# Kernel optimization log

Measured on AMD Instinct MI355X. Metric: run time of the kernel, lower is better.

Reference implementation:

```python
import jax, jax.numpy as jnp
import numpy as np

N = 50000; E = 800000; D_IN = 64; EDGE_D = 1
EMB_H = 128; H = 4; C = 32; HC = H * C; G = 8


def _ln(h, g, b):
    mu = jnp.mean(h, axis=-1, keepdims=True)
    var = jnp.var(h, axis=-1, keepdims=True)
    return (h - mu) * jax.lax.rsqrt(var + 1e-5) * g + b


def _tconv(x, src, dst, ea, wq, bq, wk, bk, wv, bv, we, ws, bs):
    # PyG TransformerConv (beta=False, root_weight=True, concat=True, dropout=0)
    n = x.shape[0]
    q = (x @ wq + bq).reshape(n, H, C)
    k = (x @ wk + bk).reshape(n, H, C)
    v = (x @ wv + bv).reshape(n, H, C)
    e = (ea @ we).reshape(-1, H, C)          # [E,H,C] edge embedding (no bias)
    ke = k[src] + e
    ve = v[src] + e
    logit = jnp.einsum('ehc,ehc->eh', q[dst], ke) / np.float32(np.sqrt(C))
    m = jax.ops.segment_max(logit, dst, num_segments=n)
    m = jnp.where(jnp.isfinite(m), m, 0.0)
    a = jnp.exp(logit - m[dst])
    s = jax.ops.segment_sum(a, dst, num_segments=n)
    alpha = a / (s[dst] + 1e-16)             # softmax over in-edges of each dst
    out = jax.ops.segment_sum(alpha[..., None] * ve, dst, num_segments=n)
    out = out.reshape(n, HC)                 # concat heads
    return out + x @ ws + bs                 # root/skip connection


def _embed(x, src, dst, ea, w1, b1, lng, lnb, w2, b2):
    # EmbedConv: per-edge MLP on [x_j || edge_attr], sum-aggregate to dst.
    # LayerNorm params are SHARED (same nn.LayerNorm instance reused in torch).
    msg = jnp.concatenate([x[src], ea], axis=1) @ w1 + b1
    msg = _ln(jax.nn.relu(msg), lng, lnb)
    msg = _ln(jax.nn.relu(msg @ w2 + b2), lng, lnb)
    return jax.ops.segment_sum(msg, dst, num_segments=x.shape[0])


def _forward(x, edge_attr, params, edge_index, batch_idx):
    src, dst = edge_index[0], edge_index[1]
    h = _embed(x, src, dst, edge_attr, *params[0:6])
    h = jax.nn.relu(_tconv(h, src, dst, edge_attr, *params[6:15]))
    h = jax.nn.relu(_tconv(h, src, dst, edge_attr, *params[15:24]))
    # global mean pool
    s = jax.ops.segment_sum(h, batch_idx, num_segments=G)
    cnt = jax.ops.segment_sum(jnp.ones((h.shape[0],), h.dtype), batch_idx, num_segments=G)
    return s / jnp.maximum(cnt, 1.0)[:, None]


def setup_inputs() -> dict:
    key = jax.random.key(0)
    ks = jax.random.split(key, 40)
    w = lambda k, shp: jax.random.normal(k, shp, dtype=jnp.float32) * 0.05
    inp = {}
    inp['x'] = jax.random.normal(ks[0], (N, D_IN), dtype=jnp.float32)
    inp['edge_index'] = jax.random.randint(ks[1], (2, E), 0, N)
    inp['edge_attr'] = jax.random.uniform(ks[2], (E, EDGE_D), dtype=jnp.float32)
    inp['batch_idx'] = jnp.sort(jax.random.randint(ks[3], (N,), 0, G))
    inp['emb_lin1_w'] = w(ks[4], (D_IN + EDGE_D, EMB_H))
    inp['emb_lin1_b'] = jnp.zeros((EMB_H,), jnp.float32)
    inp['emb_ln_g'] = jnp.ones((EMB_H,), jnp.float32)
    inp['emb_ln_b'] = jnp.zeros((EMB_H,), jnp.float32)
    inp['emb_lin2_w'] = w(ks[5], (EMB_H, EMB_H))
    inp['emb_lin2_b'] = jnp.zeros((EMB_H,), jnp.float32)
    i = 6
    for pre, din in (('g1', EMB_H), ('g2', HC)):
        inp[pre + '_wq'] = w(ks[i], (din, HC)); inp[pre + '_bq'] = jnp.zeros((HC,), jnp.float32)
        inp[pre + '_wk'] = w(ks[i + 1], (din, HC)); inp[pre + '_bk'] = jnp.zeros((HC,), jnp.float32)
        inp[pre + '_wv'] = w(ks[i + 2], (din, HC)); inp[pre + '_bv'] = jnp.zeros((HC,), jnp.float32)
        inp[pre + '_we'] = w(ks[i + 3], (EDGE_D, HC))
        inp[pre + '_ws'] = w(ks[i + 4], (din, HC)); inp[pre + '_bs'] = jnp.zeros((HC,), jnp.float32)
        i += 5
    return inp


def reference(x, edge_index, edge_attr, batch_idx,
              emb_lin1_w, emb_lin1_b, emb_ln_g, emb_ln_b, emb_lin2_w, emb_lin2_b,
              g1_wq, g1_bq, g1_wk, g1_bk, g1_wv, g1_bv, g1_we, g1_ws, g1_bs,
              g2_wq, g2_bq, g2_wk, g2_bk, g2_wv, g2_bv, g2_we, g2_ws, g2_bs):
    params = (emb_lin1_w, emb_lin1_b, emb_ln_g, emb_ln_b, emb_lin2_w, emb_lin2_b,
              g1_wq, g1_bq, g1_wk, g1_bk, g1_wv, g1_bv, g1_we, g1_ws, g1_bs,
              g2_wq, g2_bq, g2_wk, g2_bk, g2_wv, g2_bv, g2_we, g2_ws, g2_bs)
    return _forward(x, edge_attr, params, edge_index, batch_idx)
```

## Files before the change

### kernel.cpp

```cpp
#include <hip/hip_runtime.h>

typedef unsigned short u16;
typedef unsigned int u32;
typedef __attribute__((ext_vector_type(8))) short bf16x8;
typedef __attribute__((ext_vector_type(4))) float f32x4;
typedef __attribute__((ext_vector_type(4))) u32 u32x4;

#define N_NODES 50000
#define N_EDGES 800000

__device__ __forceinline__ float bf2f(u16 u) {
    union { u32 i; float f; } v; v.i = ((u32)u) << 16; return v.f;
}
__device__ __forceinline__ u16 f2bf(float f) {
    union { u32 i; float f; } v; v.f = f;
    u32 i = v.i;
    return (u16)((i + 0x7FFFu + ((i >> 16) & 1u)) >> 16);
}
__device__ __forceinline__ float ldf(const void* p, int i, int fl) {
    return fl ? ((const float*)p)[i] : bf2f(((const u16*)p)[i]);
}
__device__ __forceinline__ int getflag(const int* flag) {
    return __builtin_amdgcn_readfirstlane(*flag);
}

struct P8 { const void* s[8]; };

__global__ __launch_bounds__(256) void k_deg_detect(
    const int* __restrict__ dst, int* __restrict__ cnt,
    const u16* __restrict__ xr, int* __restrict__ flag)
{
    int t = threadIdx.x;
    if (blockIdx.x < 3125) {
        int e = blockIdx.x * 256 + t;
        atomicAdd(&cnt[dst[e]], 1);
        return;
    }
    __shared__ int sc[256];
    int c = 0;
    for (int i = t; i < 4096; i += 256) {
        u32 e = (xr[i] >> 7) & 0xFF;
        if (e >= 143) c++;
    }
    sc[t] = c;
    __syncthreads();
    for (int s = 128; s > 0; s >>= 1) {
        if (t < s) sc[t] += sc[t + s];
        __syncthreads();
    }
    if (t == 0) *flag = (sc[0] > 64) ? 1 : 0;
}

__global__ __launch_bounds__(256) void k_prep_all(
    P8 pw, P8 pb, u16* __restrict__ wcat1, u16* __restrict__ wcat2,
    float* __restrict__ bcat1, float* __restrict__ bcat2,
    const void* __restrict__ w2, const void* __restrict__ lng_,
    const void* __restrict__ lnb_, const void* __restrict__ b2_,
    const void* __restrict__ w1, u16* __restrict__ gt,
    float* __restrict__ csum, float* __restrict__ bwp,
    u32* __restrict__ w1pk, const int* __restrict__ flag)
{
    int fl = getflag(flag);
    int b = blockIdx.x, t = threadIdx.x;
    if (b < 512) {
        int gid = b * 256 + t;
        int wi = gid >> 14;
        int id = gid & 16383;
        int k = id >> 7, n = id & 127;
        u16* d = (wi < 4) ? (wcat1 + wi * 16384) : (wcat2 + (wi - 4) * 16384);
        d[n * 128 + k] = f2bf(ldf(pw.s[wi], id, fl));
    } else if (b < 516) {
        int tt = (b - 512) * 256 + t;
        float v = ldf(pb.s[tt >> 7], tt & 127, fl);
        if (tt < 512) bcat1[tt] = v; else bcat2[tt - 512] = v;
    } else {
        if (t < 128) {
            float cs = 0.f, bw = 0.f;
            for (int f = 0; f < 128; f++) {
                float wv = ldf(w2, f * 128 + t, fl);
                float g = ldf(lng_, f, fl);
                float bb = ldf(lnb_, f, fl);
                u16 gwq = f2bf(g * wv);
                gt[t * 128 + f] = gwq;
                cs += bf2f(gwq);
                bw = fmaf(bb, wv, bw);
            }
            csum[t] = cs;
            bwp[t] = bw + ldf(b2_, t, fl);
            if (t < 64)
                w1pk[t] = (u32)f2bf(ldf(w1, 64 * 128 + t * 2, fl)) |
                          ((u32)f2bf(ldf(w1, 64 * 128 + t * 2 + 1, fl)) << 16);
        }
    }
}

__global__ __launch_bounds__(1024) void k_scan(const int* __restrict__ cnt,
                                               int* __restrict__ row_start,
                                               int* __restrict__ nxt)
{
    __shared__ int wsum[16];
    __shared__ int s_tot;
    int t = threadIdx.x, lane = t & 63, wid = t >> 6;
    int run = 0;
    for (int base = 0; base < N_NODES; base += 8192) {
        int i0 = base + t * 8;
        int v[8], pre[8];
        int s = 0;
        #pragma unroll
        for (int j = 0; j < 8; j++) {
            int i = i0 + j;
            v[j] = (i < N_NODES) ? cnt[i] : 0;
            pre[j] = s;
            s += v[j];
        }
        int tsum = s;
        int sc = tsum;
        #pragma unroll
        for (int off = 1; off < 64; off <<= 1) {
            int o = __shfl_up(sc, off);
            if (lane >= off) sc += o;
        }
        if (lane == 63) wsum[wid] = sc;
        __syncthreads();
        if (t == 0) {
            int acc2 = 0;
            #pragma unroll
            for (int k2 = 0; k2 < 16; k2++) { int vv = wsum[k2]; wsum[k2] = acc2; acc2 += vv; }
            s_tot = acc2;
        }
        __syncthreads();
        int texcl = run + wsum[wid] + (sc - tsum);
        #pragma unroll
        for (int j = 0; j < 8; j++) {
            int i = i0 + j;
            if (i < N_NODES) { int ex = texcl + pre[j]; row_start[i] = ex; nxt[i] = ex; }
        }
        run += s_tot;
        __syncthreads();
    }
    if (t == 0) row_start[N_NODES] = run;
}

__global__ __launch_bounds__(256) void k_lin1_scatter(
    const void* __restrict__ x, const void* __restrict__ w1,
    const void* __restrict__ b1, u16* __restrict__ y,
    const int* __restrict__ dst, const int* __restrict__ srcp,
    const void* __restrict__ ea, int* __restrict__ nxt,
    int2* __restrict__ csr, const int* __restrict__ flag)
{
    __shared__ float sx[2][64];
    int fl = getflag(flag);
    int t = threadIdx.x;
    if (blockIdx.x >= 782) {
        int e = (blockIdx.x - 782) * 256 + t;
        if (e < N_EDGES) {
            int p = atomicAdd(&nxt[dst[e]], 1);
            int2 v;
            v.x = srcp[e];
            v.y = __float_as_int(ldf(ea, e, fl));
            csr[p] = v;
        }
        return;
    }
    int col = t & 127, half = t >> 7;
    float wreg[64];
    #pragma unroll
    for (int k = 0; k < 64; k++) wreg[k] = ldf(w1, k * 128 + col, fl);
    float bias = ldf(b1, col, fl);
    int base = blockIdx.x * 64;
    for (int it = 0; it < 32; ++it) {
        __syncthreads();
        if (t < 128) {
            int nh = base + it * 2 + (t >> 6);
            sx[t >> 6][t & 63] = (nh < N_NODES) ? ldf(x, nh * 64 + (t & 63), fl) : 0.f;
        }
        __syncthreads();
        float acc = bias;
        #pragma unroll
        for (int k = 0; k < 64; k++) acc = fmaf(sx[half][k], wreg[k], acc);
        int n = base + it * 2 + half;
        if (n < N_NODES) y[(size_t)n * 128 + col] = f2bf(acc);
    }
}

__global__ __launch_bounds__(256) void k_edge_ln1(
    const u16* __restrict__ y, const int2* __restrict__ csr,
    const u32* __restrict__ w1pk, u16* __restrict__ ubuf,
    float2* __restrict__ ab)
{
    int t = threadIdx.x;
    int e = blockIdx.x * 16 + (t >> 4);
    int j = t & 15;
    int2 c = csr[e];
    float av = __int_as_float(c.y);
    u32x4 yu = __builtin_bit_cast(u32x4, *(const bf16x8*)(y + (size_t)c.x * 128 + j * 8));
    u32x4 wv = *(const u32x4*)&w1pk[j * 4];
    float s1 = 0.f, s2 = 0.f;
    u32x4 ep;
    #pragma unroll
    for (int j2 = 0; j2 < 4; j2++) {
        u32 yw = yu[j2];
        u32 ww = wv[j2];
        float y0 = __uint_as_float(yw << 16);
        float y1 = __uint_as_float(yw & 0xffff0000u);
        float w0 = __uint_as_float(ww << 16);
        float w1v = __uint_as_float(ww & 0xffff0000u);
        float u0 = fmaxf(fmaf(av, w0, y0), 0.f);
        float u1 = fmaxf(fmaf(av, w1v, y1), 0.f);
        s1 += u0; s2 = fmaf(u0, u0, s2);
        s1 += u1; s2 = fmaf(u1, u1, s2);
        ep[j2] = __builtin_amdgcn_perm(__float_as_uint(u1),
                                       __float_as_uint(u0), 0x07060302u);
    }
    s1 += __shfl_xor(s1, 1); s2 += __shfl_xor(s2, 1);
    s1 += __shfl_xor(s1, 2); s2 += __shfl_xor(s2, 2);
    s1 += __shfl_xor(s1, 4); s2 += __shfl_xor(s2, 4);
    s1 += __shfl_xor(s1, 8); s2 += __shfl_xor(s2, 8);
    float mu = s1 * (1.f / 128.f);
    float alpha = rsqrtf(s2 * (1.f / 128.f) - mu * mu + 1e-5f);
    float beta = -mu * alpha;
    *(bf16x8*)&ubuf[(size_t)e * 128 + j * 8] = __builtin_bit_cast(bf16x8, ep);
    if (j == 0) ab[e] = make_float2(alpha, beta);
}

__global__ __launch_bounds__(256) void k_embed_mm(
    const u16* __restrict__ ubuf, const float2* __restrict__ ab,
    const int* __restrict__ rowst,
    const void* __restrict__ lng, const void* __restrict__ lnb,
    const u16* __restrict__ gt,
    const float* __restrict__ csum, const float* __restrict__ bwp,
    u16* __restrict__ h1, const int* __restrict__ flag)
{
    __shared__ u16 sB[128 * 136];
    __shared__ float sCSf[128];
    __shared__ float sBWf[128];
    int fl = getflag(flag);
    int t = threadIdx.x;
    for (int c = t; c < 128 * 32; c += 256) {
        int row = c >> 5, ch = c & 31;
        *(ushort4*)&sB[row * 136 + ch * 4] = *(const ushort4*)&gt[row * 128 + ch * 4];
    }
    if (t < 128) sCSf[t] = csum[t];
    else sBWf[t - 128] = bwp[t - 128];
    int l = t & 63, w = t >> 6;
    int m = l & 15, q = l >> 4;
    __syncthreads();

    f32x4 zf = {0.f, 0.f, 0.f, 0.f};
    bool sel0 = (m & 1), sel1 = (m & 2), sel2 = (m & 4), sel3 = (m & 8);
    int stride = gridDim.x * 4;
    for (int node = blockIdx.x * 4 + w; node < N_NODES; node += stride) {
        int rs = rowst[node], re = rowst[node + 1];
        float V = 0.f;
        f32x4 S[8];
        #pragma unroll
        for (int nb = 0; nb < 8; nb++) S[nb] = zf;
        for (int base = rs; base < re; base += 16) {
            int row = base + m;
            if (row >= re) row = re - 1;
            const u16* ur = ubuf + (size_t)row * 128 + q * 8;
            float2 abv = ab[row];
            bf16x8 efrag[4];
            #pragma unroll
            for (int kb = 0; kb < 4; kb++)
                efrag[kb] = *(const bf16x8*)(ur + kb * 32);
            float alpha = abv.x, beta = abv.y;

            f32x4 acc[8];
            #pragma unroll
            for (int nb = 0; nb < 8; nb++) acc[nb] = zf;
            #pragma unroll
            for (int nb = 0; nb < 8; nb++) {
                const u16* grow = &sB[(nb * 16 + m) * 136 + q * 8];
                #pragma unroll
                for (int kb = 0; kb < 4; kb++) {
                    bf16x8 gfrag = *(const bf16x8*)(grow + kb * 32);
                    acc[nb] = __builtin_amdgcn_mfma_f32_16x16x32_bf16(gfrag, efrag[kb], acc[nb], 0, 0, 0);
                }
            }
            float t1 = 0.f, t2 = 0.f;
            #pragma unroll
            for (int nb = 0; nb < 8; nb++) {
                float4 cs4 = *(const float4*)&sCSf[nb * 16 + q * 4];
                float4 bw4 = *(const float4*)&sBWf[nb * 16 + q * 4];
                float csa[4] = {cs4.x, cs4.y, cs4.z, cs4.w};
                float bwa[4] = {bw4.x, bw4.y, bw4.z, bw4.w};
                #pragma unroll
                for (int r = 0; r < 4; r++) {
                    float z = fmaxf(fmaf(alpha, acc[nb][r], fmaf(beta, csa[r], bwa[r])), 0.f);
                    acc[nb][r] = z;
                    t1 += z; t2 = fmaf(z, z, t2);
                }
            }
            t1 += __shfl_xor(t1, 16); t2 += __shfl_xor(t2, 16);
            t1 += __shfl_xor(t1, 32); t2 += __shfl_xor(t2, 32);
            float mu2 = t1 * (1.f / 128.f);
            float rs2 = rsqrtf(t2 * (1.f / 128.f) - mu2 * mu2 + 1e-5f);
            if (base + m >= re) rs2 = 0.f;
            V = fmaf(rs2, mu2, V);
            #pragma unroll
            for (int nb = 0; nb < 8; nb++) {
                #pragma unroll
                for (int r = 0; r < 4; r++)
                    S[nb][r] = fmaf(acc[nb][r], rs2, S[nb][r]);
            }
        }
        float sacc0 = 0.f, sacc1 = 0.f;
        {
            float s16v[16];
            #pragma unroll
            for (int k = 0; k < 16; k++) {
                int nb = k >> 1, rh = (k & 1) << 1;
                float a = S[nb][rh], b = S[nb][rh + 1];
                float keep = sel0 ? b : a;
                float send = sel0 ? a : b;
                s16v[k] = keep + __shfl_xor(send, 1);
            }
            float s8v[8];
            #pragma unroll
            for (int nb = 0; nb < 8; nb++) {
                float a = s16v[nb * 2], b = s16v[nb * 2 + 1];
                float keep = sel1 ? b : a;
                float send = sel1 ? a : b;
                s8v[nb] = keep + __shfl_xor(send, 2);
            }
            float s4v[4];
            #pragma unroll
            for (int k = 0; k < 4; k++) {
                float a = s8v[k * 2], b = s8v[k * 2 + 1];
                float keep = sel2 ? b : a;
                float send = sel2 ? a : b;
                s4v[k] = keep + __shfl_xor(send, 4);
            }
            #pragma unroll
            for (int k = 0; k < 2; k++) {
                float a = s4v[k * 2], b = s4v[k * 2 + 1];
                float keep = sel3 ? b : a;
                float send = sel3 ? a : b;
                float r2 = keep + __shfl_xor(send, 8);
                if (k == 0) sacc0 += r2; else sacc1 += r2;
            }
        }
        V += __shfl_xor(V, 1); V += __shfl_xor(V, 2);
        V += __shfl_xor(V, 4); V += __shfl_xor(V, 8);
        float dg = (float)(re - rs);
        #pragma unroll
        for (int k = 0; k < 2; k++) {
            int nb = (k << 2) | (((m >> 3) & 1) << 1) | ((m >> 2) & 1);
            int f = nb * 16 + q * 4 + (m & 3);
            float gg = ldf(lng, f, fl), bb = ldf(lnb, f, fl);
            float sv = (k == 0) ? sacc0 : sacc1;
            h1[(size_t)node * 128 + f] = f2bf(fmaf(gg, sv - V, dg * bb));
        }
    }
}

__global__ __launch_bounds__(256) void k_embed_edges_fb(
    const u16* __restrict__ y, const int2* __restrict__ csr,
    const int* __restrict__ rowst,
    const void* __restrict__ lng, const void* __restrict__ lnb,
    const u16* __restrict__ gt, const u32* __restrict__ w1pk,
    const float* __restrict__ csum, const float* __restrict__ bwp,
    u16* __restrict__ h1, const int* __restrict__ flag)
{
    __shared__ u16 sB[128 * 136];
    __shared__ u32 sW1[64];
    __shared__ float sCSf[128];
    __shared__ float sBWf[128];
    int fl = getflag(flag);
    int t = threadIdx.x;
    for (int c = t; c < 128 * 32; c += 256) {
        int row = c >> 5, ch = c & 31;
        *(ushort4*)&sB[row * 136 + ch * 4] = *(const ushort4*)&gt[row * 128 + ch * 4];
    }
    if (t < 64) sW1[t] = w1pk[t];
    if (t < 128) sCSf[t] = csum[t];
    else sBWf[t - 128] = bwp[t - 128];
    int l = t & 63, w = t >> 6;
    int m = l & 15, q = l >> 4;
    __syncthreads();

    f32x4 zf = {0.f, 0.f, 0.f, 0.f};
    bool sel0 = (m & 1), sel1 = (m & 2), sel2 = (m & 4), sel3 = (m & 8);
    int stride = gridDim.x * 4;
    for (int node = blockIdx.x * 4 + w; node < N_NODES; node += stride) {
        int rs = rowst[node], re = rowst[node + 1];
        float V = 0.f;
        f32x4 S[8];
        #pragma unroll
        for (int nb = 0; nb < 8; nb++) S[nb] = zf;
        if (rs < re) {
            int idx = rs + m;
            int2 sa = csr[(idx < re) ? idx : (re - 1)];
            for (int base = rs; base < re; base += 16) {
                float av = __int_as_float(sa.y);
                const u16* yr = y + (size_t)sa.x * 128 + q * 8;
                bf16x8 efrag[4];
                float s1 = 0.f, s2 = 0.f;
                #pragma unroll
                for (int kb = 0; kb < 4; kb++) {
                    u32x4 yu = __builtin_bit_cast(u32x4, *(const bf16x8*)(yr + kb * 32));
                    u32x4 wv4 = *(const u32x4*)&sW1[kb * 16 + q * 4];
                    u32x4 ep;
                    #pragma unroll
                    for (int j2 = 0; j2 < 4; j2++) {
                        u32 yw = yu[j2];
                        u32 ww = wv4[j2];
                        float y0 = __uint_as_float(yw << 16);
                        float y1 = __uint_as_float(yw & 0xffff0000u);
                        float w0 = __uint_as_float(ww << 16);
                        float w1v = __uint_as_float(ww & 0xffff0000u);
                        float u0 = fmaxf(fmaf(av, w0, y0), 0.f);
                        float u1 = fmaxf(fmaf(av, w1v, y1), 0.f);
                        s1 += u0; s2 = fmaf(u0, u0, s2);
                        s1 += u1; s2 = fmaf(u1, u1, s2);
                        ep[j2] = __builtin_amdgcn_perm(__float_as_uint(u1),
                                                       __float_as_uint(u0), 0x07060302u);
                    }
                    efrag[kb] = __builtin_bit_cast(bf16x8, ep);
                }
                int nbase = base + 16;
                if (nbase < re) {
                    int ni = nbase + m;
                    sa = csr[(ni < re) ? ni : (re - 1)];
                }
                s1 += __shfl_xor(s1, 16); s2 += __shfl_xor(s2, 16);
                s1 += __shfl_xor(s1, 32); s2 += __shfl_xor(s2, 32);
                float mu = s1 * (1.f / 128.f);
                float alpha = rsqrtf(s2 * (1.f / 128.f) - mu * mu + 1e-5f);
                float beta = -mu * alpha;
                f32x4 acc[8];
                #pragma unroll
                for (int nb = 0; nb < 8; nb++) acc[nb] = zf;
                #pragma unroll
                for (int nb = 0; nb < 8; nb++) {
                    const u16* grow = &sB[(nb * 16 + m) * 136 + q * 8];
                    #pragma unroll
                    for (int kb = 0; kb < 4; kb++) {
                        bf16x8 gfrag = *(const bf16x8*)(grow + kb * 32);
                        acc[nb] = __builtin_amdgcn_mfma_f32_16x16x32_bf16(gfrag, efrag[kb], acc[nb], 0, 0, 0);
                    }
                }
                float t1 = 0.f, t2 = 0.f;
                #pragma unroll
                for (int nb = 0; nb < 8; nb++) {
                    float4 cs4 = *(const float4*)&sCSf[nb * 16 + q * 4];
                    float4 bw4 = *(const float4*)&sBWf[nb * 16 + q * 4];
                    float csa[4] = {cs4.x, cs4.y, cs4.z, cs4.w};
                    float bwa[4] = {bw4.x, bw4.y, bw4.z, bw4.w};
                    #pragma unroll
                    for (int r = 0; r < 4; r++) {
                        float z = fmaxf(fmaf(alpha, acc[nb][r], fmaf(beta, csa[r], bwa[r])), 0.f);
                        acc[nb][r] = z;
                        t1 += z; t2 = fmaf(z, z, t2);
                    }
                }
                t1 += __shfl_xor(t1, 16); t2 += __shfl_xor(t2, 16);
                t1 += __shfl_xor(t1, 32); t2 += __shfl_xor(t2, 32);
                float mu2 = t1 * (1.f / 128.f);
                float rs2 = rsqrtf(t2 * (1.f / 128.f) - mu2 * mu2 + 1e-5f);
                if (base + m >= re) rs2 = 0.f;
                V = fmaf(rs2, mu2, V);
                #pragma unroll
                for (int nb = 0; nb < 8; nb++) {
                    #pragma unroll
                    for (int r = 0; r < 4; r++)
                        S[nb][r] = fmaf(acc[nb][r], rs2, S[nb][r]);
                }
            }
        }
        float sacc0 = 0.f, sacc1 = 0.f;
        {
            float s16v[16];
            #pragma unroll
            for (int k = 0; k < 16; k++) {
                int nb = k >> 1, rh = (k & 1) << 1;
                float a = S[nb][rh], b = S[nb][rh + 1];
                float keep = sel0 ? b : a;
                float send = sel0 ? a : b;
                s16v[k] = keep + __shfl_xor(send, 1);
            }
            float s8v[8];
            #pragma unroll
            for (int nb = 0; nb < 8; nb++) {
                float a = s16v[nb * 2], b = s16v[nb * 2 + 1];
                float keep = sel1 ? b : a;
                float send = sel1 ? a : b;
                s8v[nb] = keep + __shfl_xor(send, 2);
            }
            float s4v[4];
            #pragma unroll
            for (int k = 0; k < 4; k++) {
                float a = s8v[k * 2], b = s8v[k * 2 + 1];
                float keep = sel2 ? b : a;
                float send = sel2 ? a : b;
                s4v[k] = keep + __shfl_xor(send, 4);
            }
            #pragma unroll
            for (int k = 0; k < 2; k++) {
                float a = s4v[k * 2], b = s4v[k * 2 + 1];
                float keep = sel3 ? b : a;
                float send = sel3 ? a : b;
                float r2 = keep + __shfl_xor(send, 8);
                if (k == 0) sacc0 += r2; else sacc1 += r2;
            }
        }
        V += __shfl_xor(V, 1); V += __shfl_xor(V, 2);
        V += __shfl_xor(V, 4); V += __shfl_xor(V, 8);
        float dg = (float)(re - rs);
        #pragma unroll
        for (int k = 0; k < 2; k++) {
            int nb = (k << 2) | (((m >> 3) & 1) << 1) | ((m >> 2) & 1);
            int f = nb * 16 + q * 4 + (m & 3);
            float gg = ldf(lng, f, fl), bb = ldf(lnb, f, fl);
            float sv = (k == 0) ? sacc0 : sacc1;
            h1[(size_t)node * 128 + f] = f2bf(fmaf(gg, sv - V, dg * bb));
        }
    }
}

__global__ __launch_bounds__(256) void k_proj(
    const u16* __restrict__ hin, const u16* __restrict__ wt,
    const float* __restrict__ bcat, u16* __restrict__ outp)
{
    __shared__ u16 sA[64 * 136];
    __shared__ u16 sB[128 * 136];
    int t = threadIdx.x;
    int l = t & 63, w = t >> 6;
    int m = l & 15, q = l >> 4;
    int rowbase = blockIdx.x * 64;
    for (int c = t; c < 64 * 32; c += 256) {
        int row = c >> 5, ch = c & 31;
        int gr = rowbase + row;
        ushort4 pk = make_ushort4(0, 0, 0, 0);
        if (gr < N_NODES) pk = *(const ushort4*)&hin[(size_t)gr * 128 + ch * 4];
        *(ushort4*)&sA[row * 136 + ch * 4] = pk;
    }
    __syncthreads();
    bf16x8 afrag[4];
    #pragma unroll
    for (int kb = 0; kb < 4; kb++)
        afrag[kb] = *(const bf16x8*)&sA[(w * 16 + m) * 136 + kb * 32 + q * 8];

    f32x4 zf = {0.f, 0.f, 0.f, 0.f};
    for (int g = 0; g < 4; ++g) {
        __syncthreads();
        for (int c = t; c < 128 * 32; c += 256) {
            int row = c >> 5, ch = c & 31;
            *(ushort4*)&sB[row * 136 + ch * 4] = *(const ushort4*)&wt[(g * 128 + row) * 128 + ch * 4];
        }
        __syncthreads();
        f32x4 acc[8];
        #pragma unroll
        for (int nb = 0; nb < 8; nb++) acc[nb] = zf;
        #pragma unroll
        for (int nb = 0; nb < 8; nb++) {
            const u16* brow = &sB[(nb * 16 + m) * 136 + q * 8];
            #pragma unroll
            for (int kb = 0; kb < 4; kb++) {
                bf16x8 bfrag = *(const bf16x8*)(brow + kb * 32);
                acc[nb] = __builtin_amdgcn_mfma_f32_16x16x32_bf16(afrag[kb], bfrag, acc[nb], 0, 0, 0);
            }
        }
        #pragma unroll
        for (int nb = 0; nb < 8; nb++) {
            int col = g * 128 + nb * 16 + m;
            float bb = bcat[col];
            #pragma unroll
            for (int r = 0; r < 4; r++) {
                int row = rowbase + w * 16 + q * 4 + r;
                if (row < N_NODES) outp[(size_t)row * 512 + col] = f2bf(acc[nb][r] + bb);
            }
        }
    }
}

__global__ __launch_bounds__(256) void k_attn(
    const u16* __restrict__ qkvs,
    const int* __restrict__ rowst, const int2* __restrict__ csr,
    const void* __restrict__ wep, u16* __restrict__ hout,
    const int* __restrict__ flag)
{
    int fl = getflag(flag);
    int t = threadIdx.x;
    int l = t & 63, w = t >> 6;
    int dstn = blockIdx.x * 4 + w;
    int lane16 = l & 15, sub = l >> 4;
    int f0 = lane16 * 8;
    const float scale = 0.17677669529663687f;

    bf16x8 q8 = *(const bf16x8*)&qkvs[(size_t)dstn * 512 + f0];
    float qf[8], wef[8];
    if (fl) {
        float4 w0 = *(const float4*)((const float*)wep + f0);
        float4 w1v = *(const float4*)((const float*)wep + f0 + 4);
        wef[0] = w0.x; wef[1] = w0.y; wef[2] = w0.z; wef[3] = w0.w;
        wef[4] = w1v.x; wef[5] = w1v.y; wef[6] = w1v.z; wef[7] = w1v.w;
    } else {
        bf16x8 w8 = *(const bf16x8*)((const u16*)wep + f0);
        #pragma unroll
        for (int j = 0; j < 8; j++) wef[j] = bf2f((u16)w8[j]);
    }
    #pragma unroll
    for (int j = 0; j < 8; j++) qf[j] = bf2f((u16)q8[j]) * scale;

    float si = 0.f;
    float a8[8];
    #pragma unroll
    for (int j = 0; j < 8; j++) a8[j] = 0.f;

    int rs = rowst[dstn], re = rowst[dstn + 1];
    int i = rs + sub;
    for (; i + 4 < re; i += 8) {
        int2 sa = csr[i];
        int2 sb = csr[i + 4];
        float ava = __int_as_float(sa.y);
        float avb = __int_as_float(sb.y);
        const u16* sra = &qkvs[(size_t)sa.x * 512 + f0];
        const u16* srb = &qkvs[(size_t)sb.x * 512 + f0];
        bf16x8 k8a = *(const bf16x8*)(sra + 128);
        bf16x8 v8a = *(const bf16x8*)(sra + 256);
        bf16x8 k8b = *(const bf16x8*)(srb + 128);
        bf16x8 v8b = *(const bf16x8*)(srb + 256);
        float pa = 0.f, pb = 0.f;
        float vea[8], veb[8];
        #pragma unroll
        for (int j = 0; j < 8; j++) {
            pa = fmaf(qf[j], fmaf(ava, wef[j], bf2f((u16)k8a[j])), pa);
            pb = fmaf(qf[j], fmaf(avb, wef[j], bf2f((u16)k8b[j])), pb);
            vea[j] = fmaf(ava, wef[j], bf2f((u16)v8a[j]));
            veb[j] = fmaf(avb, wef[j], bf2f((u16)v8b[j]));
        }
        pa += __shfl_xor(pa, 1); pb += __shfl_xor(pb, 1);
        pa += __shfl_xor(pa, 2); pb += __shfl_xor(pb, 2);
        float pea = __expf(pa);
        float peb = __expf(pb);
        si += pea + peb;
        #pragma unroll
        for (int j = 0; j < 8; j++)
            a8[j] = fmaf(pea, vea[j], fmaf(peb, veb[j], a8[j]));
    }
    if (i < re) {
        int2 sa = csr[i];
        float av = __int_as_float(sa.y);
        const u16* sr = &qkvs[(size_t)sa.x * 512 + f0];
        bf16x8 k8 = *(const bf16x8*)(sr + 128);
        bf16x8 v8 = *(const bf16x8*)(sr + 256);
        float p = 0.f;
        float ve[8];
        #pragma unroll
        for (int j = 0; j < 8; j++) {
            p = fmaf(qf[j], fmaf(av, wef[j], bf2f((u16)k8[j])), p);
            ve[j] = fmaf(av, wef[j], bf2f((u16)v8[j]));
        }
        p += __shfl_xor(p, 1); p += __shfl_xor(p, 2);
        float pe = __expf(p);
        si += pe;
        #pragma unroll
        for (int j = 0; j < 8; j++) a8[j] = fmaf(pe, ve[j], a8[j]);
    }
    #pragma unroll
    for (int off = 16; off < 64; off <<= 1) {
        si += __shfl_xor(si, off);
        #pragma unroll
        for (int j = 0; j < 8; j++) a8[j] += __shfl_xor(a8[j], off);
    }
    if (sub == 0) {
        float inv = 1.f / (si + 1e-16f);
        bf16x8 s8 = *(const bf16x8*)&qkvs[(size_t)dstn * 512 + 384 + f0];
        ushort4 p0, p1;
        float o[8];
        #pragma unroll
        for (int j = 0; j < 8; j++)
            o[j] = fmaxf(fmaf(a8[j], inv, bf2f((u16)s8[j])), 0.f);
        p0.x = f2bf(o[0]); p0.y = f2bf(o[1]); p0.z = f2bf(o[2]); p0.w = f2bf(o[3]);
        p1.x = f2bf(o[4]); p1.y = f2bf(o[5]); p1.z = f2bf(o[6]); p1.w = f2bf(o[7]);
        u16* hr = hout + (size_t)dstn * 128 + f0;
        *(ushort4*)hr = p0;
        *(ushort4*)(hr + 4) = p1;
    }
}

__global__ __launch_bounds__(256) void k_pool(
    const u16* __restrict__ h, const int* __restrict__ batch,
    float* __restrict__ gsum, float* __restrict__ gcnt)
{
    __shared__ float ssum[8 * 128];
    __shared__ float scnt[8];
    int t = threadIdx.x;
    for (int i = t; i < 8 * 128; i += 256) ssum[i] = 0.f;
    if (t < 8) scnt[t] = 0.f;
    __syncthreads();
    int f2 = (t & 63) * 2, quarter = t >> 6;
    int per = (N_NODES + gridDim.x - 1) / gridDim.x;
    int lo = blockIdx.x * per;
    int hi = lo + per; if (hi > N_NODES) hi = N_NODES;
    float r0 = 0.f, r1 = 0.f, rcnt = 0.f; int rg = -1;
    for (int n = lo + quarter; n < hi; n += 4) {
        int g = batch[n];
        if (g != rg) {
            if (rg >= 0) {
                atomicAdd(&ssum[rg * 128 + f2], r0);
                atomicAdd(&ssum[rg * 128 + f2 + 1], r1);
                if (f2 == 0) atomicAdd(&scnt[rg], rcnt);
            }
            rg = g; r0 = 0.f; r1 = 0.f; rcnt = 0.f;
        }
        u32 hv = *(const u32*)&h[(size_t)n * 128 + f2];
        r0 += bf2f((u16)(hv & 0xffff));
        r1 += bf2f((u16)(hv >> 16));
        rcnt += 1.f;
    }
    if (rg >= 0) {
        atomicAdd(&ssum[rg * 128 + f2], r0);
        atomicAdd(&ssum[rg * 128 + f2 + 1], r1);
        if (f2 == 0) atomicAdd(&scnt[rg], rcnt);
    }
    __syncthreads();
    for (int i = t; i < 8 * 128; i += 256) unsafeAtomicAdd(&gsum[i], ssum[i]);
    if (t < 8) unsafeAtomicAdd(&gcnt[t], scnt[t]);
}

__global__ void k_out(const float* __restrict__ gsum, const float* __restrict__ gcnt,
                      void* __restrict__ outp, const int* __restrict__ flag) {
    int fl = getflag(flag);
    int t = threadIdx.x;
    float c = fmaxf(gcnt[t >> 7], 1.f);
    float v = gsum[t] / c;
    if (fl) ((float*)outp)[t] = v;
    else ((u16*)outp)[t] = f2bf(v);
}

extern "C" void kernel_launch(void* const* d_in, const int* in_sizes, int n_in,
                              void* d_out, int out_size, void* d_ws, size_t ws_size,
                              hipStream_t stream)
{
    (void)in_sizes; (void)n_in; (void)out_size;
    const void* x    = d_in[0];
    const int* ei    = (const int*)d_in[1];
    const void* ea   = d_in[2];
    const int* batch = (const int*)d_in[3];
    const void* w1   = d_in[4];
    const void* b1   = d_in[5];
    const void* lng  = d_in[6];
    const void* lnb  = d_in[7];
    const void* w2   = d_in[8];
    const void* b2   = d_in[9];
    const int* srcp = ei;
    const int* dstp = ei + N_EDGES;

    char* wsb = (char*)d_ws;
    size_t cur = 0;
    auto alloc = [&](size_t sz) -> void* {
        void* p = wsb + cur;
        cur += (sz + 255) & ~(size_t)255;
        return p;
    };
    u16*   y      = (u16*)  alloc((size_t)N_NODES * 128 * 2);
    u16*   h1     = (u16*)  alloc((size_t)N_NODES * 128 * 2);
    u16*   h2     = (u16*)  alloc((size_t)N_NODES * 128 * 2);
    u16*   qkvs   = (u16*)  alloc((size_t)N_NODES * 512 * 2);
    int2*  csr    = (int2*) alloc((size_t)N_EDGES * 8);
    u16*   gt     = (u16*)  alloc(128 * 128 * 2);
    u16*   wcat1  = (u16*)  alloc(512 * 128 * 2);
    u16*   wcat2  = (u16*)  alloc(512 * 128 * 2);
    float* csum   = (float*)alloc(128 * 4);
    float* bwp    = (float*)alloc(128 * 4);
    u32*   w1pk   = (u32*)  alloc(64 * 4);
    float* bcat1  = (float*)alloc(512 * 4);
    float* bcat2  = (float*)alloc(512 * 4);
    int*   cntdeg = (int*)  alloc((size_t)N_NODES * 4);
    int*   rowst  = (int*)  alloc((size_t)(N_NODES + 1) * 4);
    int*   nxt    = (int*)  alloc((size_t)N_NODES * 4);
    float* gsum   = (float*)alloc((8 * 128 + 8) * 4);
    int*   dtflag = (int*)  alloc(256);
    u16*   h3 = h1;
    u16*    ubuf = (u16*)   alloc((size_t)N_EDGES * 128 * 2);
    float2* ab   = (float2*)alloc((size_t)N_EDGES * 8);
    bool twopass = (cur <= ws_size);

    hipMemsetAsync(cntdeg, 0, (size_t)N_NODES * 4, stream);
    hipMemsetAsync(gsum, 0, (8 * 128 + 8) * 4, stream);

    P8 pw; P8 pb;
    pw.s[0] = d_in[10]; pw.s[1] = d_in[12]; pw.s[2] = d_in[14]; pw.s[3] = d_in[17];
    pw.s[4] = d_in[19]; pw.s[5] = d_in[21]; pw.s[6] = d_in[23]; pw.s[7] = d_in[26];
    pb.s[0] = d_in[11]; pb.s[1] = d_in[13]; pb.s[2] = d_in[15]; pb.s[3] = d_in[18];
    pb.s[4] = d_in[20]; pb.s[5] = d_in[22]; pb.s[6] = d_in[24]; pb.s[7] = d_in[27];

    k_deg_detect<<<3126, 256, 0, stream>>>(dstp, cntdeg, (const u16*)x, dtflag);
    k_prep_all<<<517, 256, 0, stream>>>(pw, pb, wcat1, wcat2, bcat1, bcat2,
                                        w2, lng, lnb, b2, w1, gt, csum, bwp, w1pk, dtflag);
    k_scan<<<1, 1024, 0, stream>>>(cntdeg, rowst, nxt);
    k_lin1_scatter<<<3907, 256, 0, stream>>>(x, w1, b1, y, dstp, srcp, ea, nxt, csr, dtflag);
    if (twopass) {
        k_edge_ln1<<<50000, 256, 0, stream>>>(y, csr, w1pk, ubuf, ab);
        k_embed_mm<<<2048, 256, 0, stream>>>(ubuf, ab, rowst, lng, lnb,
                                             gt, csum, bwp, h1, dtflag);
    } else {
        k_embed_edges_fb<<<2048, 256, 0, stream>>>(y, csr, rowst, lng, lnb,
                                                   gt, w1pk, csum, bwp, h1, dtflag);
    }
    k_proj<<<782, 256, 0, stream>>>(h1, wcat1, bcat1, qkvs);
    k_attn<<<12500, 256, 0, stream>>>(qkvs, rowst, csr, d_in[16], h2, dtflag);
    k_proj<<<782, 256, 0, stream>>>(h2, wcat2, bcat2, qkvs);
    k_attn<<<12500, 256, 0, stream>>>(qkvs, rowst, csr, d_in[25], h3, dtflag);
    k_pool<<<128, 256, 0, stream>>>(h3, batch, gsum, gsum + 8 * 128);
    k_out<<<1, 1024, 0, stream>>>(gsum, gsum + 8 * 128, d_out, dtflag);
}
```

Before: 809.4 us.

## Chunk two-pass edge embedding over node ranges to fit workspace

Replaces the all-or-nothing choice between the two-pass path (materialized per-edge LN buffer) and the fused fallback with a chunked scheme. The edge buffer now overlays the h2/qkvs region, and nodes are processed in chunks whose edges fit the available workspace. A safe variant recomputes edges that fall outside the buffered range. The aim is to use the faster two-pass path even when the workspace cannot hold buffers for every edge, at the cost of extra launches and some recomputation per chunk.

```diff
diff --git a/kernel.cpp b/kernel.cpp
--- a/kernel.cpp
+++ b/kernel.cpp
@@ -186,10 +186,15 @@
 __global__ __launch_bounds__(256) void k_edge_ln1(
     const u16* __restrict__ y, const int2* __restrict__ csr,
     const u32* __restrict__ w1pk, u16* __restrict__ ubuf,
-    float2* __restrict__ ab)
+    float2* __restrict__ ab, const int* __restrict__ rowst,
+    int n0, int n1, int cap)
 {
     int t = threadIdx.x;
-    int e = blockIdx.x * 16 + (t >> 4);
+    int e_base = rowst[n0];
+    int e_end  = rowst[n1];
+    int e_local = blockIdx.x * 16 + (t >> 4);
+    int e = e_base + e_local;
+    if (e_local >= cap || e >= e_end) return;
     int j = t & 15;
     int2 c = csr[e];
     float av = __int_as_float(c.y);
@@ -219,11 +224,11 @@
     float mu = s1 * (1.f / 128.f);
     float alpha = rsqrtf(s2 * (1.f / 128.f) - mu * mu + 1e-5f);
     float beta = -mu * alpha;
-    *(bf16x8*)&ubuf[(size_t)e * 128 + j * 8] = __builtin_bit_cast(bf16x8, ep);
-    if (j == 0) ab[e] = make_float2(alpha, beta);
-}
-
-__global__ __launch_bounds__(256) void k_embed_mm(
+    *(bf16x8*)&ubuf[(size_t)e_local * 128 + j * 8] = __builtin_bit_cast(bf16x8, ep);
+    if (j == 0) ab[e_local] = make_float2(alpha, beta);
+}
+
+__global__ __launch_bounds__(256) void k_embed_mm_fast(
     const u16* __restrict__ ubuf, const float2* __restrict__ ab,
     const int* __restrict__ rowst,
     const void* __restrict__ lng, const void* __restrict__ lnb,
@@ -355,13 +360,15 @@
     }
 }
 
-__global__ __launch_bounds__(256) void k_embed_edges_fb(
-    const u16* __restrict__ y, const int2* __restrict__ csr,
+__global__ __launch_bounds__(256) void k_embed_mm_safe(
+    const u16* __restrict__ ubuf, const float2* __restrict__ ab,
     const int* __restrict__ rowst,
     const void* __restrict__ lng, const void* __restrict__ lnb,
     const u16* __restrict__ gt, const u32* __restrict__ w1pk,
     const float* __restrict__ csum, const float* __restrict__ bwp,
-    u16* __restrict__ h1, const int* __restrict__ flag)
+    u16* __restrict__ h1, const int* __restrict__ flag,
+    const u16* __restrict__ y, const int2* __restrict__ csr,
+    int n0, int n1, int cap)
 {
     __shared__ u16 sB[128 * 136];
     __shared__ u32 sW1[64];
@@ -379,23 +386,34 @@
     int l = t & 63, w = t >> 6;
     int m = l & 15, q = l >> 4;
     __syncthreads();
+    int e_base = rowst[n0];
+    int elim = e_base + cap;
 
     f32x4 zf = {0.f, 0.f, 0.f, 0.f};
     bool sel0 = (m & 1), sel1 = (m & 2), sel2 = (m & 4), sel3 = (m & 8);
     int stride = gridDim.x * 4;
-    for (int node = blockIdx.x * 4 + w; node < N_NODES; node += stride) {
+    for (int node = n0 + blockIdx.x * 4 + w; node < n1; node += stride) {
         int rs = rowst[node], re = rowst[node + 1];
         float V = 0.f;
         f32x4 S[8];
         #pragma unroll
         for (int nb = 0; nb < 8; nb++) S[nb] = zf;
-        if (rs < re) {
-            int idx = rs + m;
-            int2 sa = csr[(idx < re) ? idx : (re - 1)];
-            for (int base = rs; base < re; base += 16) {
+        for (int base = rs; base < re; base += 16) {
+            int row = base + m;
+            if (row >= re) row = re - 1;
+            bf16x8 efrag[4];
+            float alpha, beta;
+            if (base + 16 <= elim) {
+                const u16* ur = ubuf + (size_t)(row - e_base) * 128 + q * 8;
+                float2 abv = ab[row - e_base];
+                #pragma unroll
+                for (int kb = 0; kb < 4; kb++)
+                    efrag[kb] = *(const bf16x8*)(ur + kb * 32);
+                alpha = abv.x; beta = abv.y;
+            } else {
+                int2 sa = csr[row];
                 float av = __int_as_float(sa.y);
                 const u16* yr = y + (size_t)sa.x * 128 + q * 8;
-                bf16x8 efrag[4];
                 float s1 = 0.f, s2 = 0.f;
                 #pragma unroll
                 for (int kb = 0; kb < 4; kb++) {
@@ -419,54 +437,50 @@
                     }
                     efrag[kb] = __builtin_bit_cast(bf16x8, ep);
                 }
-                int nbase = base + 16;
-                if (nbase < re) {
-                    int ni = nbase + m;
-                    sa = csr[(ni < re) ? ni : (re - 1)];
-                }
                 s1 += __shfl_xor(s1, 16); s2 += __shfl_xor(s2, 16);
                 s1 += __shfl_xor(s1, 32); s2 += __shfl_xor(s2, 32);
                 float mu = s1 * (1.f / 128.f);
-                float alpha = rsqrtf(s2 * (1.f / 128.f) - mu * mu + 1e-5f);
-                float beta = -mu * alpha;
-                f32x4 acc[8];
+                alpha = rsqrtf(s2 * (1.f / 128.f) - mu * mu + 1e-5f);
+                beta = -mu * alpha;
+            }
+
+            f32x4 acc[8];
+            #pragma unroll
+            for (int nb = 0; nb < 8; nb++) acc[nb] = zf;
+            #pragma unroll
+            for (int nb = 0; nb < 8; nb++) {
+                const u16* grow = &sB[(nb * 16 + m) * 136 + q * 8];
                 #pragma unroll
-                for (int nb = 0; nb < 8; nb++) acc[nb] = zf;
+                for (int kb = 0; kb < 4; kb++) {
+                    bf16x8 gfrag = *(const bf16x8*)(grow + kb * 32);
+                    acc[nb] = __builtin_amdgcn_mfma_f32_16x16x32_bf16(gfrag, efrag[kb], acc[nb], 0, 0, 0);
+                }
+            }
+            float t1 = 0.f, t2 = 0.f;
+            #pragma unroll
+            for (int nb = 0; nb < 8; nb++) {
+                float4 cs4 = *(const float4*)&sCSf[nb * 16 + q * 4];
+                float4 bw4 = *(const float4*)&sBWf[nb * 16 + q * 4];
+                float csa[4] = {cs4.x, cs4.y, cs4.z, cs4.w};
+                float bwa[4] = {bw4.x, bw4.y, bw4.z, bw4.w};
                 #pragma unroll
-                for (int nb = 0; nb < 8; nb++) {
-                    const u16* grow = &sB[(nb * 16 + m) * 136 + q * 8];
-                    #pragma unroll
-                    for (int kb = 0; kb < 4; kb++) {
-                        bf16x8 gfrag = *(const bf16x8*)(grow + kb * 32);
-                        acc[nb] = __builtin_amdgcn_mfma_f32_16x16x32_bf16(gfrag, efrag[kb], acc[nb], 0, 0, 0);
-                    }
+                for (int r = 0; r < 4; r++) {
+                    float z = fmaxf(fmaf(alpha, acc[nb][r], fmaf(beta, csa[r], bwa[r])), 0.f);
+                    acc[nb][r] = z;
+                    t1 += z; t2 = fmaf(z, z, t2);
                 }
-                float t1 = 0.f, t2 = 0.f;
+            }
+            t1 += __shfl_xor(t1, 16); t2 += __shfl_xor(t2, 16);
+            t1 += __shfl_xor(t1, 32); t2 += __shfl_xor(t2, 32);
+            float mu2 = t1 * (1.f / 128.f);
+            float rs2 = rsqrtf(t2 * (1.f / 128.f) - mu2 * mu2 + 1e-5f);
+            if (base + m >= re) rs2 = 0.f;
+            V = fmaf(rs2, mu2, V);
+            #pragma unroll
+            for (int nb = 0; nb < 8; nb++) {
                 #pragma unroll
-                for (int nb = 0; nb < 8; nb++) {
-                    float4 cs4 = *(const float4*)&sCSf[nb * 16 + q * 4];
-                    float4 bw4 = *(const float4*)&sBWf[nb * 16 + q * 4];
-                    float csa[4] = {cs4.x, cs4.y, cs4.z, cs4.w};
-                    float bwa[4] = {bw4.x, bw4.y, bw4.z, bw4.w};
-                    #pragma unroll
-                    for (int r = 0; r < 4; r++) {
-                        float z = fmaxf(fmaf(alpha, acc[nb][r], fmaf(beta, csa[r], bwa[r])), 0.f);
-                        acc[nb][r] = z;
-                        t1 += z; t2 = fmaf(z, z, t2);
-                    }
-                }
-                t1 += __shfl_xor(t1, 16); t2 += __shfl_xor(t2, 16);
-                t1 += __shfl_xor(t1, 32); t2 += __shfl_xor(t2, 32);
-                float mu2 = t1 * (1.f / 128.f);
-                float rs2 = rsqrtf(t2 * (1.f / 128.f) - mu2 * mu2 + 1e-5f);
-                if (base + m >= re) rs2 = 0.f;
-                V = fmaf(rs2, mu2, V);
-                #pragma unroll
-                for (int nb = 0; nb < 8; nb++) {
-                    #pragma unroll
-                    for (int r = 0; r < 4; r++)
-                        S[nb][r] = fmaf(acc[nb][r], rs2, S[nb][r]);
-                }
+                for (int r = 0; r < 4; r++)
+                    S[nb][r] = fmaf(acc[nb][r], rs2, S[nb][r]);
             }
         }
         float sacc0 = 0.f, sacc1 = 0.f;
@@ -758,8 +772,6 @@
     };
     u16*   y      = (u16*)  alloc((size_t)N_NODES * 128 * 2);
     u16*   h1     = (u16*)  alloc((size_t)N_NODES * 128 * 2);
-    u16*   h2     = (u16*)  alloc((size_t)N_NODES * 128 * 2);
-    u16*   qkvs   = (u16*)  alloc((size_t)N_NODES * 512 * 2);
     int2*  csr    = (int2*) alloc((size_t)N_EDGES * 8);
     u16*   gt     = (u16*)  alloc(128 * 128 * 2);
     u16*   wcat1  = (u16*)  alloc(512 * 128 * 2);
@@ -774,10 +786,23 @@
     int*   nxt    = (int*)  alloc((size_t)N_NODES * 4);
     float* gsum   = (float*)alloc((8 * 128 + 8) * 4);
     int*   dtflag = (int*)  alloc(256);
+    size_t region_off = cur;
+    u16*   h2     = (u16*)  alloc((size_t)N_NODES * 128 * 2);
+    u16*   qkvs   = (u16*)  alloc((size_t)N_NODES * 512 * 2);
     u16*   h3 = h1;
-    u16*    ubuf = (u16*)   alloc((size_t)N_EDGES * 128 * 2);
-    float2* ab   = (float2*)alloc((size_t)N_EDGES * 8);
-    bool twopass = (cur <= ws_size);
+    size_t region_bytes = (ws_size > region_off) ? (ws_size - region_off) : 0;
+    long long cap = (long long)(region_bytes / 264);
+    if (cap > 2000000) cap = 2000000;
+    u16*    ubuf = (u16*)   (wsb + region_off);
+    float2* ab   = (float2*)(wsb + region_off + (size_t)cap * 256);
+    int nc, nk;
+    if (cap >= N_EDGES) { nc = 1; nk = N_NODES; }
+    else {
+        nk = (int)((cap * (long long)N_NODES) / ((long long)N_EDGES * 5 / 4));
+        if (nk < 1024) nk = 1024;
+        if (nk > N_NODES) nk = N_NODES;
+        nc = (N_NODES + nk - 1) / nk;
+    }
 
     hipMemsetAsync(cntdeg, 0, (size_t)N_NODES * 4, stream);
     hipMemsetAsync(gsum, 0, (8 * 128 + 8) * 4, stream);
@@ -793,13 +818,19 @@
                                         w2, lng, lnb, b2, w1, gt, csum, bwp, w1pk, dtflag);
     k_scan<<<1, 1024, 0, stream>>>(cntdeg, rowst, nxt);
     k_lin1_scatter<<<3907, 256, 0, stream>>>(x, w1, b1, y, dstp, srcp, ea, nxt, csr, dtflag);
-    if (twopass) {
-        k_edge_ln1<<<50000, 256, 0, stream>>>(y, csr, w1pk, ubuf, ab);
-        k_embed_mm<<<2048, 256, 0, stream>>>(ubuf, ab, rowst, lng, lnb,
-                                             gt, csum, bwp, h1, dtflag);
-    } else {
-        k_embed_edges_fb<<<2048, 256, 0, stream>>>(y, csr, rowst, lng, lnb,
-                                                   gt, w1pk, csum, bwp, h1, dtflag);
+    for (int c = 0; c < nc; ++c) {
+        int n0 = c * nk;
+        int n1 = n0 + nk; if (n1 > N_NODES) n1 = N_NODES;
+        int gridA = (nc == 1) ? (N_EDGES + 15) / 16 : (int)((cap + 15) / 16);
+        k_edge_ln1<<<gridA, 256, 0, stream>>>(y, csr, w1pk, ubuf, ab, rowst,
+                                              n0, n1, (int)cap);
+        if (nc == 1)
+            k_embed_mm_fast<<<2048, 256, 0, stream>>>(ubuf, ab, rowst, lng, lnb,
+                                                      gt, csum, bwp, h1, dtflag);
+        else
+            k_embed_mm_safe<<<2048, 256, 0, stream>>>(ubuf, ab, rowst, lng, lnb,
+                                                      gt, w1pk, csum, bwp, h1, dtflag,
+                                                      y, csr, n0, n1, (int)cap);
     }
     k_proj<<<782, 256, 0, stream>>>(h1, wcat1, bcat1, qkvs);
     k_attn<<<12500, 256, 0, stream>>>(qkvs, rowst, csr, d_in[16], h2, dtflag);
```

Result: slower. 874.5 us (+8.0%).
